# Kernel tuning notes

Hardware: AMD Instinct MI355X
Metric: run time of the kernel (lower is better)

## Reference

```python
import jax, jax.numpy as jnp
import numpy as np

N, E = 50000, 800000
IN_D, HID, OUT = 256, 128, 64
EPS = 1e-5


def _gcn(x, src, dst, W, b, n):
    # PyG GCNConv: x@W, add self-loops, sym-normalize, scatter-sum, +b
    h = x @ W
    loops = jnp.arange(n, dtype=src.dtype)
    s = jnp.concatenate([src, loops])
    d = jnp.concatenate([dst, loops])
    deg = jax.ops.segment_sum(jnp.ones_like(d, dtype=h.dtype), d, num_segments=n)
    dinv = jnp.where(deg > 0, jax.lax.rsqrt(deg), 0.0)
    norm = dinv[s] * dinv[d]  # [E+N]
    msg = h[s] * norm[:, None]  # gather + scale, [E+N, F]
    return jax.ops.segment_sum(msg, d, num_segments=n) + b


def _bn(y, g, be):
    # training-mode BatchNorm1d: biased batch stats
    mu = jnp.mean(y, axis=0)
    var = jnp.mean((y - mu) ** 2, axis=0)
    return g * (y - mu) * jax.lax.rsqrt(var + EPS) + be


def setup_inputs() -> dict:
    key = jax.random.key(0)
    ks = jax.random.split(key, 12)
    sc = lambda i, o: 1.0 / np.sqrt(i)
    inp = {
        "x": jax.random.normal(ks[0], (N, IN_D), jnp.float32),
        "edge_index": jax.random.randint(ks[1], (2, E), 0, N, jnp.int32),
        "W_emb": jax.random.normal(ks[2], (IN_D, HID), jnp.float32) * sc(IN_D, HID),
        "b_emb": jnp.zeros((HID,), jnp.float32),
        "W_g1": jax.random.normal(ks[3], (HID, HID), jnp.float32) * sc(HID, HID),
        "b_g1": jnp.zeros((HID,), jnp.float32),
        "W_g2": jax.random.normal(ks[4], (HID, OUT), jnp.float32) * sc(HID, OUT),
        "b_g2": jnp.zeros((OUT,), jnp.float32),
        "W_m0": jax.random.normal(ks[5], (2 * OUT, OUT), jnp.float32) * sc(2 * OUT, OUT),
        "b_m0": jnp.zeros((OUT,), jnp.float32),
        "g_m0": jnp.ones((OUT,), jnp.float32),
        "be_m0": jnp.zeros((OUT,), jnp.float32),
        "W_m1": jax.random.normal(ks[6], (OUT, OUT // 2), jnp.float32) * sc(OUT, OUT // 2),
        "b_m1": jnp.zeros((OUT // 2,), jnp.float32),
        "g_m1": jnp.ones((OUT // 2,), jnp.float32),
        "be_m1": jnp.zeros((OUT // 2,), jnp.float32),
        "W_m2": jax.random.normal(ks[7], (OUT // 2, 1), jnp.float32) * sc(OUT // 2, 1),
        "b_m2": jnp.zeros((1,), jnp.float32),
    }
    return inp


def reference(x, edge_index, W_emb, b_emb, W_g1, b_g1, W_g2, b_g2,
              W_m0, b_m0, g_m0, be_m0, W_m1, b_m1, g_m1, be_m1, W_m2, b_m2):
    src, dst = edge_index[0], edge_index[1]
    n = x.shape[0]
    h = x @ W_emb + b_emb                       # embedding (dropout = eval identity)
    h = jax.nn.relu(_gcn(h, src, dst, W_g1, b_g1, n))
    h = _gcn(h, src, dst, W_g2, b_g2, n)        # [N, OUT]
    # edge-endpoint gather + concat -> [E, 2*OUT]
    ls = jnp.concatenate([h[src], h[dst]], axis=1)
    ls = jax.nn.relu(_bn(ls @ W_m0 + b_m0, g_m0, be_m0))
    ls = jax.nn.relu(_bn(ls @ W_m1 + b_m1, g_m1, be_m1))
    ls = ls @ W_m2 + b_m2
    return jax.nn.sigmoid(ls)                   # [E, 1]
```

## Files before the change

### kernel.cpp

```cpp
#include <hip/hip_runtime.h>
#include <math.h>

static constexpr int IN_D = 256;
static constexpr int HIDD = 128;

__global__ void init_kernel(int* __restrict__ hist, int* __restrict__ odeg,
                            double* __restrict__ dsum, int n) {
    int i = blockIdx.x * 256 + threadIdx.x;
    if (i < n) { hist[i] = 0; odeg[i] = 0; }
    if (i < 256) dsum[i] = 0.0;
}

__global__ void hist_kernel(const int* __restrict__ src, const int* __restrict__ dst,
                            int* __restrict__ hist, int* __restrict__ odeg, int E) {
    int e = blockIdx.x * 256 + threadIdx.x;
    if (e < E) {
        atomicAdd(&hist[dst[e]], 1);
        atomicAdd(&odeg[src[e]], 1);
    }
}

__global__ __launch_bounds__(256)
void blocksum_kernel(const int* __restrict__ hist, int* __restrict__ bsum, int N) {
    __shared__ int red[256];
    const int t = threadIdx.x;
    int i = blockIdx.x * 256 + t;
    red[t] = (i < N) ? hist[i] : 0;
    __syncthreads();
#pragma unroll
    for (int off = 128; off > 0; off >>= 1) {
        if (t < off) red[t] += red[t + off];
        __syncthreads();
    }
    if (t == 0) bsum[blockIdx.x] = red[0];
}

__global__ __launch_bounds__(256)
void scanb_kernel(int* __restrict__ bsum, int NB) {
    __shared__ int s[256];
    const int t = threadIdx.x;
    int v = (t < NB) ? bsum[t] : 0;
    s[t] = v;
    __syncthreads();
#pragma unroll
    for (int off = 1; off < 256; off <<= 1) {
        int u = (t >= off) ? s[t - off] : 0;
        __syncthreads();
        s[t] += u;
        __syncthreads();
    }
    if (t < NB) bsum[t] = s[t] - v;
}

__global__ __launch_bounds__(256)
void prefix_kernel(const int* __restrict__ hist, const int* __restrict__ bsum,
                   int* __restrict__ rowptr, int* __restrict__ cursor,
                   float* __restrict__ dinv, int N, int E) {
    __shared__ int s[256];
    const int t = threadIdx.x;
    int i = blockIdx.x * 256 + t;
    int v = (i < N) ? hist[i] : 0;
    s[t] = v;
    __syncthreads();
#pragma unroll
    for (int off = 1; off < 256; off <<= 1) {
        int u = (t >= off) ? s[t - off] : 0;
        __syncthreads();
        s[t] += u;
        __syncthreads();
    }
    if (i < N) {
        int run = bsum[blockIdx.x] + s[t] - v;
        rowptr[i] = run;
        cursor[i] = run;
        dinv[i] = rsqrtf((float)v + 1.0f);
    }
    if (blockIdx.x == 0 && t == 0) rowptr[N] = E;
}

__global__ void fill_kernel(const int* __restrict__ src, const int* __restrict__ dst,
                            int* __restrict__ cursor, int* __restrict__ ssort,
                            int* __restrict__ dsort, int* __restrict__ esort, int E) {
    int e = blockIdx.x * 256 + threadIdx.x;
    if (e < E) {
        int d = dst[e];
        int pos = atomicAdd(&cursor[d], 1);
        ssort[pos] = src[e];
        dsort[pos] = d;
        esort[pos] = e;
    }
}

template <int K, int NCOL, bool RELU, bool BIAS>
__global__ __launch_bounds__((NCOL / 4) * 16)
void mm_kernel(const float* __restrict__ A, const float* __restrict__ W,
               const float* __restrict__ bias, float* __restrict__ C, int M) {
    constexpr int MT = 64;
    constexpr int KK = 32;
    constexpr int TPB = (NCOL / 4) * (MT / 4);
    __shared__ float xs[KK][MT + 4];
    __shared__ float ws[KK][NCOL];

    const int t = threadIdx.x;
    const int m0 = blockIdx.x * MT;
    const int tc = t % (NCOL / 4);
    const int tr = t / (NCOL / 4);
    const int c0 = tc * 4, r0 = tr * 4;

    float acc[4][4] = {};

    for (int ko = 0; ko < K; ko += KK) {
        constexpr int NF4 = MT * KK / 4;
        for (int idx = t; idx < NF4; idx += TPB) {
            int m = idx >> 3;
            int jk = idx & 7;
            float4 v = make_float4(0.f, 0.f, 0.f, 0.f);
            if (m0 + m < M)
                v = *(const float4*)&A[(size_t)(m0 + m) * K + ko + jk * 4];
            if (RELU) {
                v.x = fmaxf(v.x, 0.f); v.y = fmaxf(v.y, 0.f);
                v.z = fmaxf(v.z, 0.f); v.w = fmaxf(v.w, 0.f);
            }
            xs[jk * 4 + 0][m] = v.x;
            xs[jk * 4 + 1][m] = v.y;
            xs[jk * 4 + 2][m] = v.z;
            xs[jk * 4 + 3][m] = v.w;
        }
        constexpr int WF4 = KK * NCOL / 4;
        const float4* Wp = (const float4*)(W + (size_t)ko * NCOL);
        float4* wsp = (float4*)&ws[0][0];
        for (int idx = t; idx < WF4; idx += TPB) wsp[idx] = Wp[idx];
        __syncthreads();

#pragma unroll
        for (int kk = 0; kk < KK; kk++) {
            float4 av = *(const float4*)&xs[kk][r0];
            float4 wv = *(const float4*)&ws[kk][c0];
            acc[0][0] += av.x * wv.x; acc[0][1] += av.x * wv.y;
            acc[0][2] += av.x * wv.z; acc[0][3] += av.x * wv.w;
            acc[1][0] += av.y * wv.x; acc[1][1] += av.y * wv.y;
            acc[1][2] += av.y * wv.z; acc[1][3] += av.y * wv.w;
            acc[2][0] += av.z * wv.x; acc[2][1] += av.z * wv.y;
            acc[2][2] += av.z * wv.z; acc[2][3] += av.z * wv.w;
            acc[3][0] += av.w * wv.x; acc[3][1] += av.w * wv.y;
            acc[3][2] += av.w * wv.z; acc[3][3] += av.w * wv.w;
        }
        __syncthreads();
    }

    float4 b4 = make_float4(0.f, 0.f, 0.f, 0.f);
    if (BIAS) b4 = *(const float4*)&bias[c0];
#pragma unroll
    for (int i = 0; i < 4; i++) {
        int row = m0 + r0 + i;
        if (row < M) {
            float4 o;
            o.x = acc[i][0] + b4.x; o.y = acc[i][1] + b4.y;
            o.z = acc[i][2] + b4.z; o.w = acc[i][3] + b4.w;
            *(float4*)&C[(size_t)row * NCOL + c0] = o;
        }
    }
}

template <int NC>
__global__ __launch_bounds__(256)
void agg_kernel(const float* __restrict__ hW, const float* __restrict__ dinv,
                const int* __restrict__ rowptr, const int* __restrict__ src_sorted,
                const float* __restrict__ b, float* __restrict__ agg, int N) {
    constexpr int TPN = NC / 4;
    constexpr int NPB = 256 / TPN;
    const int t = threadIdx.x;
    const int node = blockIdx.x * NPB + t / TPN;
    if (node >= N) return;
    const int c4 = (t % TPN) * 4;

    const float dn = dinv[node];
    float4 h = *(const float4*)&hW[(size_t)node * NC + c4];
    float4 bb = *(const float4*)&b[c4];
    float4 acc;
    acc.x = h.x * dn * dn + bb.x;
    acc.y = h.y * dn * dn + bb.y;
    acc.z = h.z * dn * dn + bb.z;
    acc.w = h.w * dn * dn + bb.w;

    const int i1 = rowptr[node + 1];
    for (int i = rowptr[node]; i < i1; i++) {
        int s = src_sorted[i];
        float w = dinv[s] * dn;
        float4 v = *(const float4*)&hW[(size_t)s * NC + c4];
        acc.x += v.x * w; acc.y += v.y * w; acc.z += v.z * w; acc.w += v.w * w;
    }
    *(float4*)&agg[(size_t)node * NC + c4] = acc;
}

__global__ void concat_w_kernel(const float* __restrict__ Wm0, float* __restrict__ Wc) {
    int i = blockIdx.x * 256 + threadIdx.x;
    if (i < 64 * 128) {
        int k = i >> 7, j = i & 127;
        Wc[i] = (j < 64) ? Wm0[k * 64 + j] : Wm0[(64 + k) * 64 + (j - 64)];
    }
}

__global__ __launch_bounds__(256)
void bn0_node_kernel(const float* __restrict__ AB, const int* __restrict__ ideg,
                     const int* __restrict__ odeg, const int* __restrict__ rowptr,
                     const int* __restrict__ ssort,
                     double* __restrict__ dS1, double* __restrict__ dS2,
                     double* __restrict__ dX, int N) {
    const int t = threadIdx.x;
    const int c4 = (t & 15) * 4;
    const int slot = t >> 4;
    float rS1[4] = {}, rS2[4] = {}, rX[4] = {};

    for (int n = blockIdx.x * 16 + slot; n < N; n += gridDim.x * 16) {
        float od = (float)odeg[n];
        float id = (float)ideg[n];
        float4 A4 = *(const float4*)&AB[(size_t)n * 128 + c4];
        float4 B4 = *(const float4*)&AB[(size_t)n * 128 + 64 + c4];
        float4 ca = make_float4(0.f, 0.f, 0.f, 0.f);
        const int i1 = rowptr[n + 1];
        for (int i = rowptr[n]; i < i1; i++) {
            int s = ssort[i];
            float4 v = *(const float4*)&AB[(size_t)s * 128 + c4];
            ca.x += v.x; ca.y += v.y; ca.z += v.z; ca.w += v.w;
        }
        rS1[0] += od * A4.x + id * B4.x;
        rS1[1] += od * A4.y + id * B4.y;
        rS1[2] += od * A4.z + id * B4.z;
        rS1[3] += od * A4.w + id * B4.w;
        rS2[0] += od * A4.x * A4.x + id * B4.x * B4.x;
        rS2[1] += od * A4.y * A4.y + id * B4.y * B4.y;
        rS2[2] += od * A4.z * A4.z + id * B4.z * B4.z;
        rS2[3] += od * A4.w * A4.w + id * B4.w * B4.w;
        rX[0] += ca.x * B4.x; rX[1] += ca.y * B4.y;
        rX[2] += ca.z * B4.z; rX[3] += ca.w * B4.w;
    }

    __shared__ float m1[16][64], m2[16][64], mx[16][64];
#pragma unroll
    for (int i = 0; i < 4; i++) {
        m1[slot][c4 + i] = rS1[i];
        m2[slot][c4 + i] = rS2[i];
        mx[slot][c4 + i] = rX[i];
    }
    __syncthreads();
    if (t < 64) {
        float a1 = 0.f, a2 = 0.f, ax = 0.f;
#pragma unroll
        for (int q = 0; q < 16; q++) { a1 += m1[q][t]; a2 += m2[q][t]; ax += mx[q][t]; }
        atomicAdd(&dS1[t], (double)a1);
        atomicAdd(&dS2[t], (double)a2);
        atomicAdd(&dX[t], (double)ax);
    }
}

__global__ void bnprep0_kernel(const double* __restrict__ dS1, const double* __restrict__ dS2,
                               const double* __restrict__ dX,
                               const float* __restrict__ g, const float* __restrict__ be,
                               const float* __restrict__ bm,
                               float* __restrict__ s0, float* __restrict__ t0, int E) {
    int c = threadIdx.x;
    if (c < 64) {
        double a1 = dS1[c] / (double)E;
        double var = (dS2[c] + 2.0 * dX[c]) / (double)E - a1 * a1;
        double mean = a1 + (double)bm[c];
        double inv = 1.0 / sqrt(var + 1e-5);
        float s = (float)((double)g[c] * inv);
        float t = (float)((double)be[c] - (double)s * mean);
        s0[c] = s; t0[c] = t;
    }
}

__global__ __launch_bounds__(512)
void mlp1_fused_kernel(const float* __restrict__ AB, const int* __restrict__ ssort,
                       const int* __restrict__ dsort, const float* __restrict__ bm0v,
                       const float* __restrict__ s0v, const float* __restrict__ t0v,
                       const float* __restrict__ Wm1, const float* __restrict__ bm1,
                       float* __restrict__ z1, double* __restrict__ st, int E) {
    constexpr int TE = 256;
    __shared__ float smem[64 * TE];
    __shared__ float wls[64 * 32];
    __shared__ float svls[64], tvls[64], bmls[64], b1ls[32];

    const int t = threadIdx.x;
    for (int i = t; i < 2048; i += 512) wls[i] = Wm1[i];
    if (t < 64) { svls[t] = s0v[t]; tvls[t] = t0v[t]; bmls[t] = bm0v[t]; }
    if (t < 32) b1ls[t] = bm1[t];
    __syncthreads();

    const int base = blockIdx.x * TE;
    const int le = t >> 1, half = t & 1;
    const int pos = base + le;
    if (pos < E) {
        const int s = ssort[pos], d = dsort[pos];
        const float* Ar = AB + (size_t)s * 128;
        const float* Br = AB + (size_t)d * 128 + 64;
#pragma unroll
        for (int q = 0; q < 8; q++) {
            int c = half * 32 + q * 4;
            float4 a = *(const float4*)&Ar[c];
            float4 b = *(const float4*)&Br[c];
            float4 sv = *(const float4*)&svls[c];
            float4 tv = *(const float4*)&tvls[c];
            float4 mv = *(const float4*)&bmls[c];
            smem[(c + 0) * TE + le] = fmaxf(sv.x * (a.x + b.x + mv.x) + tv.x, 0.f);
            smem[(c + 1) * TE + le] = fmaxf(sv.y * (a.y + b.y + mv.y) + tv.y, 0.f);
            smem[(c + 2) * TE + le] = fmaxf(sv.z * (a.z + b.z + mv.z) + tv.z, 0.f);
            smem[(c + 3) * TE + le] = fmaxf(sv.w * (a.w + b.w + mv.w) + tv.w, 0.f);
        }
    } else {
#pragma unroll
        for (int q = 0; q < 8; q++) {
            int c = half * 32 + q * 4;
            smem[(c + 0) * TE + le] = 0.f; smem[(c + 1) * TE + le] = 0.f;
            smem[(c + 2) * TE + le] = 0.f; smem[(c + 3) * TE + le] = 0.f;
        }
    }
    __syncthreads();

    const int tr = t >> 3, tc = t & 7;
    const int r0 = tr * 4, c0 = tc * 4;
    float acc[4][4];
#pragma unroll
    for (int i = 0; i < 4; i++) {
        acc[i][0] = b1ls[c0 + 0]; acc[i][1] = b1ls[c0 + 1];
        acc[i][2] = b1ls[c0 + 2]; acc[i][3] = b1ls[c0 + 3];
    }
#pragma unroll 8
    for (int kk = 0; kk < 64; kk++) {
        float4 av = *(const float4*)&smem[kk * TE + r0];
        float4 wv = *(const float4*)&wls[kk * 32 + c0];
        acc[0][0] += av.x * wv.x; acc[0][1] += av.x * wv.y;
        acc[0][2] += av.x * wv.z; acc[0][3] += av.x * wv.w;
        acc[1][0] += av.y * wv.x; acc[1][1] += av.y * wv.y;
        acc[1][2] += av.y * wv.z; acc[1][3] += av.y * wv.w;
        acc[2][0] += av.z * wv.x; acc[2][1] += av.z * wv.y;
        acc[2][2] += av.z * wv.z; acc[2][3] += av.z * wv.w;
        acc[3][0] += av.w * wv.x; acc[3][1] += av.w * wv.y;
        acc[3][2] += av.w * wv.z; acc[3][3] += av.w * wv.w;
    }

    float cs1[4] = {0.f, 0.f, 0.f, 0.f};
    float cs2[4] = {0.f, 0.f, 0.f, 0.f};
#pragma unroll
    for (int i = 0; i < 4; i++) {
        int pz = base + r0 + i;
        if (pz < E) {
            float4 o;
            o.x = acc[i][0]; o.y = acc[i][1]; o.z = acc[i][2]; o.w = acc[i][3];
            *(float4*)&z1[(size_t)pz * 32 + c0] = o;
            cs1[0] += o.x; cs1[1] += o.y; cs1[2] += o.z; cs1[3] += o.w;
            cs2[0] += o.x * o.x; cs2[1] += o.y * o.y;
            cs2[2] += o.z * o.z; cs2[3] += o.w * o.w;
        }
    }
    __syncthreads();
    float* ls1 = smem;
    float* ls2 = smem + 64 * 32;
    ls1[tr * 32 + c0 + 0] = cs1[0]; ls1[tr * 32 + c0 + 1] = cs1[1];
    ls1[tr * 32 + c0 + 2] = cs1[2]; ls1[tr * 32 + c0 + 3] = cs1[3];
    ls2[tr * 32 + c0 + 0] = cs2[0]; ls2[tr * 32 + c0 + 1] = cs2[1];
    ls2[tr * 32 + c0 + 2] = cs2[2]; ls2[tr * 32 + c0 + 3] = cs2[3];
    __syncthreads();
    if (t < 32) {
        float a1 = 0.f, a2 = 0.f;
#pragma unroll
        for (int r = 0; r < 64; r++) { a1 += ls1[r * 32 + t]; a2 += ls2[r * 32 + t]; }
        atomicAdd(&st[t], (double)a1);
        atomicAdd(&st[32 + t], (double)a2);
    }
}

__global__ void bnprep1_kernel(const double* __restrict__ st,
                               const float* __restrict__ g, const float* __restrict__ be,
                               float* __restrict__ s1, float* __restrict__ t1, int E) {
    int c = threadIdx.x;
    if (c < 32) {
        double mu = st[c] / (double)E;
        double var = st[32 + c] / (double)E - mu * mu;
        double inv = 1.0 / sqrt(var + 1e-5);
        float s = (float)((double)g[c] * inv);
        float t = (float)((double)be[c] - (double)s * mu);
        s1[c] = s; t1[c] = t;
    }
}

__global__ void mlp2_kernel(const float* __restrict__ z1, const int* __restrict__ esort,
                            const float* __restrict__ s1, const float* __restrict__ t1,
                            const float* __restrict__ Wm2, const float* __restrict__ bm2,
                            float* __restrict__ out, int E) {
    int pos = blockIdx.x * 256 + threadIdx.x;
    if (pos >= E) return;
    const float* zr = z1 + (size_t)pos * 32;
    float acc = bm2[0];
#pragma unroll
    for (int k = 0; k < 32; k += 4) {
        float4 z4 = *(const float4*)&zr[k];
        float4 sv = *(const float4*)&s1[k];
        float4 tv = *(const float4*)&t1[k];
        float4 wv = *(const float4*)&Wm2[k];
        acc += fmaxf(sv.x * z4.x + tv.x, 0.f) * wv.x;
        acc += fmaxf(sv.y * z4.y + tv.y, 0.f) * wv.y;
        acc += fmaxf(sv.z * z4.z + tv.z, 0.f) * wv.z;
        acc += fmaxf(sv.w * z4.w + tv.w, 0.f) * wv.w;
    }
    out[esort[pos]] = 1.f / (1.f + expf(-acc));
}

extern "C" void kernel_launch(void* const* d_in, const int* in_sizes, int n_in,
                              void* d_out, int out_size, void* d_ws, size_t ws_size,
                              hipStream_t stream) {
    const float* x      = (const float*)d_in[0];
    const int*   eidx   = (const int*)d_in[1];
    const float* W_emb  = (const float*)d_in[2];
    const float* b_emb  = (const float*)d_in[3];
    const float* W_g1   = (const float*)d_in[4];
    const float* b_g1   = (const float*)d_in[5];
    const float* W_g2   = (const float*)d_in[6];
    const float* b_g2   = (const float*)d_in[7];
    const float* W_m0   = (const float*)d_in[8];
    const float* b_m0   = (const float*)d_in[9];
    const float* g_m0   = (const float*)d_in[10];
    const float* be_m0  = (const float*)d_in[11];
    const float* W_m1   = (const float*)d_in[12];
    const float* b_m1   = (const float*)d_in[13];
    const float* g_m1   = (const float*)d_in[14];
    const float* be_m1  = (const float*)d_in[15];
    const float* W_m2   = (const float*)d_in[16];
    const float* b_m2   = (const float*)d_in[17];
    float* out = (float*)d_out;

    const int N = in_sizes[0] / IN_D;
    const int E = in_sizes[1] / 2;
    const int* src = eidx;
    const int* dst = eidx + E;

    char* p = (char*)d_ws;
    auto alloc = [&](size_t bytes) {
        void* r = (void*)p;
        p += (bytes + 255) & ~(size_t)255;
        return r;
    };
    int*    hist   = (int*)alloc((size_t)N * 4);
    int*    odeg   = (int*)alloc((size_t)N * 4);
    int*    rowptr = (int*)alloc((size_t)(N + 1) * 4);
    int*    cursor = (int*)alloc((size_t)N * 4);
    int*    bsum   = (int*)alloc(256 * 4);
    int*    ssort  = (int*)alloc((size_t)E * 4);
    int*    dsort  = (int*)alloc((size_t)E * 4);
    int*    esort  = (int*)alloc((size_t)E * 4);
    float*  dinv   = (float*)alloc((size_t)N * 4);
    float*  B2     = (float*)alloc((size_t)N * HIDD * 4);
    float*  B3     = (float*)alloc((size_t)N * HIDD * 4);
    float*  B4     = (float*)alloc((size_t)N * HIDD * 4);
    float*  z1     = (float*)alloc((size_t)E * 32 * 4);
    float*  Wc     = (float*)alloc(64 * 128 * 4);
    double* dsum   = (double*)alloc(256 * 8);
    float*  s0     = (float*)alloc(64 * 4);
    float*  t0     = (float*)alloc(64 * 4);
    float*  s1v    = (float*)alloc(32 * 4);
    float*  t1v    = (float*)alloc(32 * 4);

    double* dS1 = dsum;
    double* dS2 = dsum + 64;
    double* dX  = dsum + 128;
    double* st1 = dsum + 192;

    float* h0   = B2;  float* agg2 = B2;
    float* hW1  = B3;  float* hW2  = B3;
    float* agg1 = B4;  float* AB   = B4;

    const int nbE = (E + 255) / 256;
    const int nbN = (N + 255) / 256;

    init_kernel<<<nbN, 256, 0, stream>>>(hist, odeg, dsum, N);
    hist_kernel<<<nbE, 256, 0, stream>>>(src, dst, hist, odeg, E);
    blocksum_kernel<<<nbN, 256, 0, stream>>>(hist, bsum, N);
    scanb_kernel<<<1, 256, 0, stream>>>(bsum, nbN);
    prefix_kernel<<<nbN, 256, 0, stream>>>(hist, bsum, rowptr, cursor, dinv, N, E);
    fill_kernel<<<nbE, 256, 0, stream>>>(src, dst, cursor, ssort, dsort, esort, E);

    mm_kernel<256, 128, false, true><<<(N + 63) / 64, 512, 0, stream>>>(x, W_emb, b_emb, h0, N);

    mm_kernel<128, 128, false, false><<<(N + 63) / 64, 512, 0, stream>>>(h0, W_g1, nullptr, hW1, N);
    agg_kernel<128><<<(N + 7) / 8, 256, 0, stream>>>(hW1, dinv, rowptr, ssort, b_g1, agg1, N);

    mm_kernel<128, 64, true, false><<<(N + 63) / 64, 256, 0, stream>>>(agg1, W_g2, nullptr, hW2, N);
    agg_kernel<64><<<(N + 15) / 16, 256, 0, stream>>>(hW2, dinv, rowptr, ssort, b_g2, agg2, N);

    concat_w_kernel<<<32, 256, 0, stream>>>(W_m0, Wc);
    mm_kernel<64, 128, false, false><<<(N + 63) / 64, 512, 0, stream>>>(agg2, Wc, nullptr, AB, N);

    bn0_node_kernel<<<512, 256, 0, stream>>>(AB, hist, odeg, rowptr, ssort, dS1, dS2, dX, N);
    bnprep0_kernel<<<1, 64, 0, stream>>>(dS1, dS2, dX, g_m0, be_m0, b_m0, s0, t0, E);

    mlp1_fused_kernel<<<(E + 255) / 256, 512, 0, stream>>>(AB, ssort, dsort, b_m0,
                                                           s0, t0, W_m1, b_m1, z1, st1, E);
    bnprep1_kernel<<<1, 32, 0, stream>>>(st1, g_m1, be_m1, s1v, t1v, E);

    mlp2_kernel<<<nbE, 256, 0, stream>>>(z1, esort, s1v, t1v, W_m2, b_m2, out, E);
}
```

Measured before the change: 694.8 us.

## Unroll neighbor gathers by two and halve mlp1 shared tile via two-phase K

The CSR gather loops in the GCN aggregation and BN0 node-stats kernels now process two neighbors per iteration, so two independent row loads are in flight at once. The fused mlp1 kernel's staging buffer shrinks from 64x256 to 32x256 floats by splitting the K=64 reduction into two phases of 32, with an extra barrier between them. The bias is added at the end instead of being used to initialise the accumulators. Cutting LDS use roughly in half (about 74KB to about 42KB) should allow more resident blocks per CU, at the cost of one more synchronisation and staging pass per block.

```diff
diff --git a/kernel.cpp b/kernel.cpp
--- a/kernel.cpp
+++ b/kernel.cpp
@@ -183,8 +183,21 @@
     acc.z = h.z * dn * dn + bb.z;
     acc.w = h.w * dn * dn + bb.w;
 
+    int i = rowptr[node];
     const int i1 = rowptr[node + 1];
-    for (int i = rowptr[node]; i < i1; i++) {
+    for (; i + 2 <= i1; i += 2) {
+        int sa = src_sorted[i];
+        int sb = src_sorted[i + 1];
+        float wa = dinv[sa] * dn;
+        float wb = dinv[sb] * dn;
+        float4 va = *(const float4*)&hW[(size_t)sa * NC + c4];
+        float4 vb = *(const float4*)&hW[(size_t)sb * NC + c4];
+        acc.x += va.x * wa + vb.x * wb;
+        acc.y += va.y * wa + vb.y * wb;
+        acc.z += va.z * wa + vb.z * wb;
+        acc.w += va.w * wa + vb.w * wb;
+    }
+    if (i < i1) {
         int s = src_sorted[i];
         float w = dinv[s] * dn;
         float4 v = *(const float4*)&hW[(size_t)s * NC + c4];
@@ -218,8 +231,16 @@
         float4 A4 = *(const float4*)&AB[(size_t)n * 128 + c4];
         float4 B4 = *(const float4*)&AB[(size_t)n * 128 + 64 + c4];
         float4 ca = make_float4(0.f, 0.f, 0.f, 0.f);
+        int i = rowptr[n];
         const int i1 = rowptr[n + 1];
-        for (int i = rowptr[n]; i < i1; i++) {
+        for (; i + 2 <= i1; i += 2) {
+            int sa = ssort[i], sb = ssort[i + 1];
+            float4 va = *(const float4*)&AB[(size_t)sa * 128 + c4];
+            float4 vb = *(const float4*)&AB[(size_t)sb * 128 + c4];
+            ca.x += va.x + vb.x; ca.y += va.y + vb.y;
+            ca.z += va.z + vb.z; ca.w += va.w + vb.w;
+        }
+        if (i < i1) {
             int s = ssort[i];
             float4 v = *(const float4*)&AB[(size_t)s * 128 + c4];
             ca.x += v.x; ca.y += v.y; ca.z += v.z; ca.w += v.w;
@@ -278,7 +299,7 @@
                        const float* __restrict__ Wm1, const float* __restrict__ bm1,
                        float* __restrict__ z1, double* __restrict__ st, int E) {
     constexpr int TE = 256;
-    __shared__ float smem[64 * TE];
+    __shared__ float yt[32 * TE];
     __shared__ float wls[64 * 32];
     __shared__ float svls[64], tvls[64], bmls[64], b1ls[32];
 
@@ -291,63 +312,70 @@
     const int base = blockIdx.x * TE;
     const int le = t >> 1, half = t & 1;
     const int pos = base + le;
-    if (pos < E) {
-        const int s = ssort[pos], d = dsort[pos];
-        const float* Ar = AB + (size_t)s * 128;
-        const float* Br = AB + (size_t)d * 128 + 64;
-#pragma unroll
-        for (int q = 0; q < 8; q++) {
-            int c = half * 32 + q * 4;
-            float4 a = *(const float4*)&Ar[c];
-            float4 b = *(const float4*)&Br[c];
-            float4 sv = *(const float4*)&svls[c];
-            float4 tv = *(const float4*)&tvls[c];
-            float4 mv = *(const float4*)&bmls[c];
-            smem[(c + 0) * TE + le] = fmaxf(sv.x * (a.x + b.x + mv.x) + tv.x, 0.f);
-            smem[(c + 1) * TE + le] = fmaxf(sv.y * (a.y + b.y + mv.y) + tv.y, 0.f);
-            smem[(c + 2) * TE + le] = fmaxf(sv.z * (a.z + b.z + mv.z) + tv.z, 0.f);
-            smem[(c + 3) * TE + le] = fmaxf(sv.w * (a.w + b.w + mv.w) + tv.w, 0.f);
-        }
-    } else {
-#pragma unroll
-        for (int q = 0; q < 8; q++) {
-            int c = half * 32 + q * 4;
-            smem[(c + 0) * TE + le] = 0.f; smem[(c + 1) * TE + le] = 0.f;
-            smem[(c + 2) * TE + le] = 0.f; smem[(c + 3) * TE + le] = 0.f;
-        }
-    }
-    __syncthreads();
+    const bool valid = pos < E;
+    const int s = valid ? ssort[pos] : 0;
+    const int d = valid ? dsort[pos] : 0;
+    const float* Ar = AB + (size_t)s * 128;
+    const float* Br = AB + (size_t)d * 128 + 64;
 
     const int tr = t >> 3, tc = t & 7;
     const int r0 = tr * 4, c0 = tc * 4;
-    float acc[4][4];
-#pragma unroll
-    for (int i = 0; i < 4; i++) {
-        acc[i][0] = b1ls[c0 + 0]; acc[i][1] = b1ls[c0 + 1];
-        acc[i][2] = b1ls[c0 + 2]; acc[i][3] = b1ls[c0 + 3];
-    }
+    float acc[4][4] = {};
+
+#pragma unroll
+    for (int ph = 0; ph < 2; ph++) {
+        if (ph) __syncthreads();
+        const int cb = ph * 32 + half * 16;
+        if (valid) {
+#pragma unroll
+            for (int q = 0; q < 4; q++) {
+                int c = cb + q * 4;
+                int kl = c - ph * 32;
+                float4 a = *(const float4*)&Ar[c];
+                float4 b = *(const float4*)&Br[c];
+                float4 sv = *(const float4*)&svls[c];
+                float4 tv = *(const float4*)&tvls[c];
+                float4 mv = *(const float4*)&bmls[c];
+                yt[(kl + 0) * TE + le] = fmaxf(sv.x * (a.x + b.x + mv.x) + tv.x, 0.f);
+                yt[(kl + 1) * TE + le] = fmaxf(sv.y * (a.y + b.y + mv.y) + tv.y, 0.f);
+                yt[(kl + 2) * TE + le] = fmaxf(sv.z * (a.z + b.z + mv.z) + tv.z, 0.f);
+                yt[(kl + 3) * TE + le] = fmaxf(sv.w * (a.w + b.w + mv.w) + tv.w, 0.f);
+            }
+        } else {
+#pragma unroll
+            for (int q = 0; q < 4; q++) {
+                int kl = half * 16 + q * 4;
+                yt[(kl + 0) * TE + le] = 0.f; yt[(kl + 1) * TE + le] = 0.f;
+                yt[(kl + 2) * TE + le] = 0.f; yt[(kl + 3) * TE + le] = 0.f;
+            }
+        }
+        __syncthreads();
+
 #pragma unroll 8
-    for (int kk = 0; kk < 64; kk++) {
-        float4 av = *(const float4*)&smem[kk * TE + r0];
-        float4 wv = *(const float4*)&wls[kk * 32 + c0];
-        acc[0][0] += av.x * wv.x; acc[0][1] += av.x * wv.y;
-        acc[0][2] += av.x * wv.z; acc[0][3] += av.x * wv.w;
-        acc[1][0] += av.y * wv.x; acc[1][1] += av.y * wv.y;
-        acc[1][2] += av.y * wv.z; acc[1][3] += av.y * wv.w;
-        acc[2][0] += av.z * wv.x; acc[2][1] += av.z * wv.y;
-        acc[2][2] += av.z * wv.z; acc[2][3] += av.z * wv.w;
-        acc[3][0] += av.w * wv.x; acc[3][1] += av.w * wv.y;
-        acc[3][2] += av.w * wv.z; acc[3][3] += av.w * wv.w;
+        for (int kk = 0; kk < 32; kk++) {
+            float4 av = *(const float4*)&yt[kk * TE + r0];
+            float4 wv = *(const float4*)&wls[(ph * 32 + kk) * 32 + c0];
+            acc[0][0] += av.x * wv.x; acc[0][1] += av.x * wv.y;
+            acc[0][2] += av.x * wv.z; acc[0][3] += av.x * wv.w;
+            acc[1][0] += av.y * wv.x; acc[1][1] += av.y * wv.y;
+            acc[1][2] += av.y * wv.z; acc[1][3] += av.y * wv.w;
+            acc[2][0] += av.z * wv.x; acc[2][1] += av.z * wv.y;
+            acc[2][2] += av.z * wv.z; acc[2][3] += av.z * wv.w;
+            acc[3][0] += av.w * wv.x; acc[3][1] += av.w * wv.y;
+            acc[3][2] += av.w * wv.z; acc[3][3] += av.w * wv.w;
+        }
     }
 
     float cs1[4] = {0.f, 0.f, 0.f, 0.f};
     float cs2[4] = {0.f, 0.f, 0.f, 0.f};
+    float4 bo = *(const float4*)&b1ls[c0];
 #pragma unroll
     for (int i = 0; i < 4; i++) {
         int pz = base + r0 + i;
         if (pz < E) {
             float4 o;
-            o.x = acc[i][0]; o.y = acc[i][1]; o.z = acc[i][2]; o.w = acc[i][3];
+            o.x = acc[i][0] + bo.x; o.y = acc[i][1] + bo.y;
+            o.z = acc[i][2] + bo.z; o.w = acc[i][3] + bo.w;
             *(float4*)&z1[(size_t)pz * 32 + c0] = o;
             cs1[0] += o.x; cs1[1] += o.y; cs1[2] += o.z; cs1[3] += o.w;
             cs2[0] += o.x * o.x; cs2[1] += o.y * o.y;
@@ -355,8 +383,8 @@
         }
     }
     __syncthreads();
-    float* ls1 = smem;
-    float* ls2 = smem + 64 * 32;
+    float* ls1 = yt;
+    float* ls2 = yt + 64 * 32;
     ls1[tr * 32 + c0 + 0] = cs1[0]; ls1[tr * 32 + c0 + 1] = cs1[1];
     ls1[tr * 32 + c0 + 2] = cs1[2]; ls1[tr * 32 + c0 + 3] = cs1[3];
     ls2[tr * 32 + c0 + 0] = cs2[0]; ls2[tr * 32 + c0 + 1] = cs2[1];
```

Measured after the change: 620.7 us. 1.12x faster.
